# Kernel tuning notes

Hardware: AMD Instinct MI355X
Metric: run time of the kernel (lower is better)

## Reference

```python
import jax, jax.numpy as jnp
import numpy as np

D_MODEL = 1024
D_INNER = 2048
N_EXPERTS = 8
TOP_K = 2
INIT_STD = 0.02


def setup_inputs() -> dict:
    key = jax.random.key(0)
    ks = jax.random.split(key, 6)
    B, S = 2, 2048
    x = jax.random.normal(ks[0], (B, S, D_MODEL), dtype=jnp.float32)
    router_w = jax.random.normal(ks[1], (N_EXPERTS, D_MODEL), dtype=jnp.float32) * (INIT_STD * 0.1)
    router_b = jnp.zeros((N_EXPERTS,), dtype=jnp.float32)
    gate_w = jax.random.normal(ks[2], (N_EXPERTS, D_MODEL, D_INNER), dtype=jnp.float32) * INIT_STD
    up_w = jax.random.normal(ks[3], (N_EXPERTS, D_MODEL, D_INNER), dtype=jnp.float32) * INIT_STD
    down_w = jax.random.normal(ks[4], (N_EXPERTS, D_INNER, D_MODEL), dtype=jnp.float32) * INIT_STD
    return {"x": x, "router_w": router_w, "router_b": router_b,
            "gate_w": gate_w, "up_w": up_w, "down_w": down_w}


def reference(x, router_w, router_b, gate_w, up_w, down_w):
    # Router: softmax over experts, top-k, renormalize top-k probs.
    logits = jnp.einsum('bsd,ed->bse', x, router_w) + router_b          # [B,S,E]
    probs = jax.nn.softmax(logits, axis=-1)
    top_p, top_i = jax.lax.top_k(probs, TOP_K)                           # [B,S,K]
    top_p = top_p / jnp.sum(top_p, axis=-1, keepdims=True)
    # Per-expert combine weight: c[b,s,e] = sum_k top_p[b,s,k] * [top_i[b,s,k]==e]
    onehot = jax.nn.one_hot(top_i, N_EXPERTS, dtype=x.dtype)             # [B,S,K,E]
    combine = jnp.einsum('bsk,bske->bse', top_p, onehot)                 # [B,S,E]
    # SwiGLU FFN for every expert (dense form of the masked dispatch),
    # zeroed/weighted by combine coefficients.
    g = jnp.einsum('bsd,edf->ebsf', x, gate_w)                           # [E,B,S,F]
    u = jnp.einsum('bsd,edf->ebsf', x, up_w)
    h = jax.nn.silu(g) * u
    y = jnp.einsum('ebsf,efd->ebsd', h, down_w)                          # [E,B,S,D]
    out = jnp.einsum('ebsd,bse->bsd', y, combine)
    return out
```

## Files before the change

### kernel.cpp

```cpp
#include <hip/hip_runtime.h>
#include <hip/hip_bf16.h>
#include <stdint.h>

#define D_MODEL 1024
#define D_INNER 2048
#define NEXP 8
#define TOPK 2
#define BM 128
#define MAXT 72

typedef float f32x4 __attribute__((ext_vector_type(4)));
typedef short bf16x8 __attribute__((ext_vector_type(8)));

#define MEMFENCE asm volatile("" ::: "memory")

__device__ __forceinline__ unsigned short f2b(float f) {
    union { float f; uint32_t u; } v; v.f = f;
    uint32_t u = v.u;
    return (unsigned short)((u + 0x7fffu + ((u >> 16) & 1u)) >> 16);
}

__device__ __forceinline__ void gl_lds16(const void* g, void* l) {
    __builtin_amdgcn_global_load_lds((const __attribute__((address_space(1))) void*)g,
                                     (__attribute__((address_space(3))) void*)l, 16, 0, 0);
}

__global__ __launch_bounds__(256) void cast_x_kernel(
    const float* __restrict__ in, unsigned short* __restrict__ out, int n8)
{
    int i = blockIdx.x * 256 + threadIdx.x;
    if (i >= n8) return;
    const float4* p = (const float4*)(in + (size_t)i * 8);
    float4 a = p[0], b = p[1];
    unsigned short o[8] = {f2b(a.x), f2b(a.y), f2b(a.z), f2b(a.w),
                           f2b(b.x), f2b(b.y), f2b(b.z), f2b(b.w)};
    *(uint4*)(out + (size_t)i * 8) = *(uint4*)o;
}

__global__ __launch_bounds__(256) void tcast_kernel(
    const float* __restrict__ in, unsigned short* __restrict__ out, int K, int N)
{
    __shared__ unsigned short S[64][68];
    int e = blockIdx.z;
    int n0 = blockIdx.x * 64, k0 = blockIdx.y * 64;
    const float* ib = in + (size_t)e * K * N;
    unsigned short* ob = out + (size_t)e * N * K;
    int tid = threadIdx.x;
    int kk = tid >> 4, nn4 = (tid & 15) * 4;
#pragma unroll
    for (int j = 0; j < 4; j++) {
        int k = kk + 16 * j;
        float4 v = *(const float4*)&ib[(size_t)(k0 + k) * N + n0 + nn4];
        ushort4 s; s.x = f2b(v.x); s.y = f2b(v.y); s.z = f2b(v.z); s.w = f2b(v.w);
        *(ushort4*)&S[k][nn4] = s;
    }
    __syncthreads();
    int nn = tid >> 4, kk4 = (tid & 15) * 4;
#pragma unroll
    for (int j = 0; j < 4; j++) {
        int n = nn + 16 * j;
        ushort4 s;
        s.x = S[kk4 + 0][n]; s.y = S[kk4 + 1][n];
        s.z = S[kk4 + 2][n]; s.w = S[kk4 + 3][n];
        *(ushort4*)&ob[(size_t)(n0 + n) * K + k0 + kk4] = s;
    }
}

__global__ __launch_bounds__(64) void router_kernel(
    const float* __restrict__ x, const float* __restrict__ rw,
    const float* __restrict__ rb, int* __restrict__ top_i,
    float* __restrict__ top_w, int T)
{
    int t = blockIdx.x;
    if (t >= T) return;
    int l = threadIdx.x;
    float xv[16];
#pragma unroll
    for (int i = 0; i < 16; i++) xv[i] = x[(size_t)t * D_MODEL + l + 64 * i];
    float logit[NEXP];
#pragma unroll
    for (int e = 0; e < NEXP; e++) {
        float acc = 0.f;
#pragma unroll
        for (int i = 0; i < 16; i++) acc += xv[i] * rw[e * D_MODEL + l + 64 * i];
#pragma unroll
        for (int s = 32; s > 0; s >>= 1) acc += __shfl_xor(acc, s, 64);
        logit[e] = acc + rb[e];
    }
    if (l == 0) {
        int i0 = 0; float m0 = logit[0];
#pragma unroll
        for (int e = 1; e < NEXP; e++) if (logit[e] > m0) { m0 = logit[e]; i0 = e; }
        int i1 = -1; float m1 = -3.0e38f;
#pragma unroll
        for (int e = 0; e < NEXP; e++) {
            if (e == i0) continue;
            if (logit[e] > m1) { m1 = logit[e]; i1 = e; }
        }
        float w0 = 1.f / (1.f + expf(m1 - m0));
        top_i[t * 2 + 0] = i0; top_i[t * 2 + 1] = i1;
        top_w[t * 2 + 0] = w0; top_w[t * 2 + 1] = 1.f - w0;
    }
}

__global__ __launch_bounds__(256) void bucket_kernel(
    const int* __restrict__ top_i, const float* __restrict__ top_w,
    int* __restrict__ meta, int* __restrict__ tok_of_slot,
    float* __restrict__ w_of_slot, int T)
{
    __shared__ int cnt[256][NEXP];
    __shared__ int pre[256][NEXP];
    __shared__ int tot[NEXP];
    __shared__ int off[NEXP + 1];
    int tid = threadIdx.x;
    int per = (T + 255) / 256;
    int t0 = tid * per;
    for (int e = 0; e < NEXP; e++) cnt[tid][e] = 0;
    for (int t = t0; t < t0 + per && t < T; t++)
        for (int k = 0; k < TOPK; k++) cnt[tid][top_i[t * 2 + k]]++;
    __syncthreads();
    if (tid < NEXP) {
        int run = 0;
        for (int i = 0; i < 256; i++) { pre[i][tid] = run; run += cnt[i][tid]; }
        tot[tid] = run;
    }
    __syncthreads();
    if (tid == 0) {
        off[0] = 0;
        for (int e = 0; e < NEXP; e++) off[e + 1] = off[e] + tot[e];
        for (int e = 0; e <= NEXP; e++) meta[e] = off[e];
        int nt = 0;
        for (int e = 0; e < NEXP; e++)
            for (int r = off[e]; r < off[e + 1]; r += BM)
                meta[16 + nt++] = (e << 16) | r;
        for (; nt < MAXT; nt++) meta[16 + nt] = -1;
    }
    __syncthreads();
    int lc[NEXP];
#pragma unroll
    for (int e = 0; e < NEXP; e++) lc[e] = 0;
    for (int t = t0; t < t0 + per && t < T; t++) {
        for (int k = 0; k < TOPK; k++) {
            int e = top_i[t * 2 + k];
            int slot = off[e] + pre[tid][e] + lc[e]++;
            tok_of_slot[slot] = t;
            w_of_slot[slot] = top_w[t * 2 + k];
        }
    }
}

__global__ __launch_bounds__(256, 2) void moe_gate_up(
    const unsigned short* __restrict__ xb, const unsigned short* __restrict__ wgT,
    const unsigned short* __restrict__ wuT, const int* __restrict__ meta,
    const int* __restrict__ tok_of_slot, unsigned short* __restrict__ H)
{
    extern __shared__ __align__(16) unsigned short lds[];

    int lin = blockIdx.x;
    int strip = (lin & 7) * 2 + ((lin >> 3) & 1);
    int tix = lin >> 4;
    int packed = meta[16 + tix];
    if (packed < 0) return;
    int e = packed >> 16, row0 = packed & 0xffff;
    int Mloc = min(BM, meta[e + 1] - row0);
    int f0 = strip * 128;

    int tid = threadIdx.x, wv = tid >> 6, lane = tid & 63;

    const unsigned short* srcA[2];
    const unsigned short* srcG[2];
    const unsigned short* srcU[2];
#pragma unroll
    for (int j = 0; j < 2; j++) {
        int row = j * 64 + (tid >> 2);
        int p = tid & 3;
        int koffA = 8 * (p ^ ((row >> 1) & 3));
        int slot = row0 + ((row < Mloc) ? row : 0);
        srcA[j] = xb + (size_t)tok_of_slot[slot] * D_MODEL + koffA;
        size_t wb = (size_t)e * D_MODEL * D_INNER + (size_t)(f0 + row) * D_MODEL + koffA;
        srcG[j] = wgT + wb;
        srcU[j] = wuT + wb;
    }

    int wm = wv >> 1, wn = wv & 1;
    int lrow = lane & 15, kgrp = lane >> 4;
    int co = 8 * (kgrp ^ ((lrow >> 1) & 3));

    int arow[4], brow[4];
#pragma unroll
    for (int fm = 0; fm < 4; fm++) arow[fm] = (wm * 64 + fm * 16 + lrow) * 32;
#pragma unroll
    for (int fn = 0; fn < 4; fn++) brow[fn] = (wn * 64 + fn * 16 + lrow) * 32;

    f32x4 accg[4][4], accu[4][4];
#pragma unroll
    for (int i = 0; i < 4; i++)
#pragma unroll
        for (int j = 0; j < 4; j++) {
            accg[i][j] = (f32x4){0.f, 0.f, 0.f, 0.f};
            accu[i][j] = (f32x4){0.f, 0.f, 0.f, 0.f};
        }

    auto stage = [&](int u) {
        int kk = u * 32;
        unsigned short* base = lds + (u % 3) * 12288;
#pragma unroll
        for (int j = 0; j < 2; j++) {
            int d = (j * 256 + wv * 64) * 8;
            gl_lds16(srcA[j] + kk, base + d);
            gl_lds16(srcG[j] + kk, base + 4096 + d);
            gl_lds16(srcU[j] + kk, base + 8192 + d);
        }
    };

    const int NT = D_MODEL / 32;
    stage(0); stage(1);
    MEMFENCE;

    for (int t = 0; t < NT; ++t) {
        if (t + 2 < NT) stage(t + 2);
        int ahead = NT - 1 - t;
        if (ahead >= 2)      asm volatile("s_waitcnt vmcnt(12)" ::: "memory");
        else if (ahead == 1) asm volatile("s_waitcnt vmcnt(6)"  ::: "memory");
        else                 asm volatile("s_waitcnt vmcnt(0)"  ::: "memory");
        __builtin_amdgcn_s_barrier();
        MEMFENCE;

        const unsigned short* base = lds + (t % 3) * 12288;
        bf16x8 a[4], bg[4], bu[4];
#pragma unroll
        for (int fm = 0; fm < 4; fm++) a[fm] = *(const bf16x8*)(base + arow[fm] + co);
#pragma unroll
        for (int fn = 0; fn < 4; fn++) {
            bg[fn] = *(const bf16x8*)(base + 4096 + brow[fn] + co);
            bu[fn] = *(const bf16x8*)(base + 8192 + brow[fn] + co);
        }
        __builtin_amdgcn_s_setprio(1);
#pragma unroll
        for (int fm = 0; fm < 4; fm++)
#pragma unroll
            for (int fn = 0; fn < 4; fn++) {
                accg[fm][fn] = __builtin_amdgcn_mfma_f32_16x16x32_bf16(a[fm], bg[fn], accg[fm][fn], 0, 0, 0);
                accu[fm][fn] = __builtin_amdgcn_mfma_f32_16x16x32_bf16(a[fm], bu[fn], accu[fm][fn], 0, 0, 0);
            }
        __builtin_amdgcn_s_setprio(0);
        MEMFENCE;
        asm volatile("s_waitcnt lgkmcnt(0)" ::: "memory");
        __builtin_amdgcn_s_barrier();
        MEMFENCE;
    }

#pragma unroll
    for (int fm = 0; fm < 4; fm++)
#pragma unroll
        for (int fn = 0; fn < 4; fn++)
#pragma unroll
            for (int r = 0; r < 4; r++) {
                int m = wm * 64 + fm * 16 + kgrp * 4 + r;
                if (m < Mloc) {
                    int n = wn * 64 + fn * 16 + lrow;
                    float g = accg[fm][fn][r], u = accu[fm][fn][r];
                    float h = g / (1.f + __expf(-g)) * u;
                    H[(size_t)(row0 + m) * D_INNER + f0 + n] = f2b(h);
                }
            }
}

__global__ __launch_bounds__(256, 2) void moe_down(
    const unsigned short* __restrict__ H, const unsigned short* __restrict__ wdT,
    const int* __restrict__ meta, const int* __restrict__ tok_of_slot,
    const float* __restrict__ w_of_slot, float* __restrict__ out, int S2)
{
    __shared__ unsigned short lds[3 * 8192];
    __shared__ int toks[BM];
    __shared__ float wts[BM];

    int lin = blockIdx.x;
    int d0 = (lin & 7) * 128;
    int tix = lin >> 3;
    int packed = meta[16 + tix];
    if (packed < 0) return;
    int e = packed >> 16, row0 = packed & 0xffff;
    int Mloc = min(BM, meta[e + 1] - row0);

    int tid = threadIdx.x, wv = tid >> 6, lane = tid & 63;
    if (tid < BM) {
        bool v = tid < Mloc;
        toks[tid] = v ? tok_of_slot[row0 + tid] : 0;
        wts[tid] = v ? w_of_slot[row0 + tid] : 0.f;
    }

    const unsigned short* srcA[2];
    const unsigned short* srcB[2];
#pragma unroll
    for (int j = 0; j < 2; j++) {
        int row = j * 64 + (tid >> 2);
        int p = tid & 3;
        int koff = 8 * (p ^ ((row >> 1) & 3));
        int slot = min(row0 + row, S2 - 1);
        srcA[j] = H + (size_t)slot * D_INNER + koff;
        srcB[j] = wdT + (size_t)e * D_INNER * D_MODEL + (size_t)(d0 + row) * D_INNER + koff;
    }

    int wm = wv >> 1, wn = wv & 1;
    int lrow = lane & 15, kgrp = lane >> 4;
    int co = 8 * (kgrp ^ ((lrow >> 1) & 3));

    int arow[4], brow[4];
#pragma unroll
    for (int fm = 0; fm < 4; fm++) arow[fm] = (wm * 64 + fm * 16 + lrow) * 32;
#pragma unroll
    for (int fn = 0; fn < 4; fn++) brow[fn] = (wn * 64 + fn * 16 + lrow) * 32;

    f32x4 acc[4][4];
#pragma unroll
    for (int i = 0; i < 4; i++)
#pragma unroll
        for (int j = 0; j < 4; j++) acc[i][j] = (f32x4){0.f, 0.f, 0.f, 0.f};

    auto stage = [&](int u) {
        int kk = u * 32;
        unsigned short* base = lds + (u % 3) * 8192;
#pragma unroll
        for (int j = 0; j < 2; j++) {
            int d = (j * 256 + wv * 64) * 8;
            gl_lds16(srcA[j] + kk, base + d);
            gl_lds16(srcB[j] + kk, base + 4096 + d);
        }
    };

    const int NT = D_INNER / 32;
    stage(0); stage(1);
    MEMFENCE;

    for (int t = 0; t < NT; ++t) {
        if (t + 2 < NT) stage(t + 2);
        int ahead = NT - 1 - t;
        if (ahead >= 2)      asm volatile("s_waitcnt vmcnt(8)" ::: "memory");
        else if (ahead == 1) asm volatile("s_waitcnt vmcnt(4)" ::: "memory");
        else                 asm volatile("s_waitcnt vmcnt(0)" ::: "memory");
        __builtin_amdgcn_s_barrier();
        MEMFENCE;

        const unsigned short* base = lds + (t % 3) * 8192;
        bf16x8 a[4], b[4];
#pragma unroll
        for (int fm = 0; fm < 4; fm++) a[fm] = *(const bf16x8*)(base + arow[fm] + co);
#pragma unroll
        for (int fn = 0; fn < 4; fn++) b[fn] = *(const bf16x8*)(base + 4096 + brow[fn] + co);
        __builtin_amdgcn_s_setprio(1);
#pragma unroll
        for (int fm = 0; fm < 4; fm++)
#pragma unroll
            for (int fn = 0; fn < 4; fn++)
                acc[fm][fn] = __builtin_amdgcn_mfma_f32_16x16x32_bf16(a[fm], b[fn], acc[fm][fn], 0, 0, 0);
        __builtin_amdgcn_s_setprio(0);
        MEMFENCE;
        asm volatile("s_waitcnt lgkmcnt(0)" ::: "memory");
        __builtin_amdgcn_s_barrier();
        MEMFENCE;
    }

#pragma unroll
    for (int fm = 0; fm < 4; fm++)
#pragma unroll
        for (int fn = 0; fn < 4; fn++)
#pragma unroll
            for (int r = 0; r < 4; r++) {
                int m = wm * 64 + fm * 16 + kgrp * 4 + r;
                if (m < Mloc) {
                    int n = wn * 64 + fn * 16 + lrow;
                    atomicAdd(&out[(size_t)toks[m] * D_MODEL + d0 + n], wts[m] * acc[fm][fn][r]);
                }
            }
}

extern "C" void kernel_launch(void* const* d_in, const int* in_sizes, int n_in,
                              void* d_out, int out_size, void* d_ws, size_t ws_size,
                              hipStream_t stream) {
    const float* x  = (const float*)d_in[0];
    const float* rw = (const float*)d_in[1];
    const float* rb = (const float*)d_in[2];
    const float* gw = (const float*)d_in[3];
    const float* uw = (const float*)d_in[4];
    const float* dw = (const float*)d_in[5];
    float* out = (float*)d_out;

    int T = in_sizes[0] / D_MODEL;
    int S2 = 2 * T;

    char* ws = (char*)d_ws;
    size_t cur = 0;
    auto take = [&](size_t bytes) { char* p = ws + cur; cur = (cur + bytes + 255) & ~(size_t)255; return p; };
    int*   top_i = (int*)take((size_t)S2 * 4);
    float* top_w = (float*)take((size_t)S2 * 4);
    int*   meta  = (int*)take(1024);
    int*   tos   = (int*)take((size_t)S2 * 4);
    float* wos   = (float*)take((size_t)S2 * 4);
    unsigned short* xb  = (unsigned short*)take((size_t)T * D_MODEL * 2);
    unsigned short* wgT = (unsigned short*)take((size_t)NEXP * D_MODEL * D_INNER * 2);
    unsigned short* wuT = (unsigned short*)take((size_t)NEXP * D_MODEL * D_INNER * 2);
    unsigned short* wdT = (unsigned short*)take((size_t)NEXP * D_MODEL * D_INNER * 2);
    unsigned short* H   = (unsigned short*)take((size_t)S2 * D_INNER * 2);

    static const int GU_LDS = 3 * 12288 * 2;
    hipFuncSetAttribute((const void*)moe_gate_up,
                        hipFuncAttributeMaxDynamicSharedMemorySize, GU_LDS);

    hipMemsetAsync(d_out, 0, (size_t)out_size * sizeof(float), stream);

    int n8 = T * D_MODEL / 8;
    cast_x_kernel<<<(n8 + 255) / 256, 256, 0, stream>>>(x, xb, n8);
    tcast_kernel<<<dim3(D_INNER / 64, D_MODEL / 64, NEXP), 256, 0, stream>>>(gw, wgT, D_MODEL, D_INNER);
    tcast_kernel<<<dim3(D_INNER / 64, D_MODEL / 64, NEXP), 256, 0, stream>>>(uw, wuT, D_MODEL, D_INNER);
    tcast_kernel<<<dim3(D_MODEL / 64, D_INNER / 64, NEXP), 256, 0, stream>>>(dw, wdT, D_INNER, D_MODEL);

    router_kernel<<<T, 64, 0, stream>>>(x, rw, rb, top_i, top_w, T);
    bucket_kernel<<<1, 256, 0, stream>>>(top_i, top_w, meta, tos, wos, T);

    moe_gate_up<<<MAXT * 16, 256, GU_LDS, stream>>>(xb, wgT, wuT, meta, tos, H);
    moe_down<<<MAXT * 8, 256, 0, stream>>>(H, wdT, meta, tos, wos, out, S2);
}
```

Measured before the change: 273.1 us.

## Prefetch next LDS fragments, use one barrier per k-step, merge weight cast kernels

Both grouped GEMM kernels now load the next k-tile's MFMA fragments from LDS into registers right after the barrier. The MFMAs for the current tile issue first, followed by the global-to-LDS stage and a single wait-and-barrier. This drops the second per-iteration barrier and the lgkmcnt stall, at the cost of more live registers. The three weight transpose-cast launches are merged into one kernel on a 32x32x24 grid, where out-of-range blocks exit early.

After: 266.7 us. -2.4%, faster.

```diff
diff --git a/kernel.cpp b/kernel.cpp
--- a/kernel.cpp
+++ b/kernel.cpp
@@ -37,12 +37,19 @@
     *(uint4*)(out + (size_t)i * 8) = *(uint4*)o;
 }
 
-__global__ __launch_bounds__(256) void tcast_kernel(
-    const float* __restrict__ in, unsigned short* __restrict__ out, int K, int N)
+__global__ __launch_bounds__(256) void tcast3_kernel(
+    const float* __restrict__ gw, const float* __restrict__ uw, const float* __restrict__ dw,
+    unsigned short* __restrict__ gT, unsigned short* __restrict__ uT, unsigned short* __restrict__ dT)
 {
     __shared__ unsigned short S[64][68];
-    int e = blockIdx.z;
+    int which = blockIdx.z >> 3;
+    int e = blockIdx.z & 7;
+    const float* in; unsigned short* out; int K, N;
+    if (which == 0)      { in = gw; out = gT; K = D_MODEL; N = D_INNER; }
+    else if (which == 1) { in = uw; out = uT; K = D_MODEL; N = D_INNER; }
+    else                 { in = dw; out = dT; K = D_INNER; N = D_MODEL; }
     int n0 = blockIdx.x * 64, k0 = blockIdx.y * 64;
+    if (n0 >= N || k0 >= K) return;
     const float* ib = in + (size_t)e * K * N;
     unsigned short* ob = out + (size_t)e * N * K;
     int tid = threadIdx.x;
@@ -213,28 +220,28 @@
         }
     };
 
+    bf16x8 a[4], bg[4], bu[4];
+    auto load_frags = [&](int u) {
+        const unsigned short* base = lds + (u % 3) * 12288;
+#pragma unroll
+        for (int fm = 0; fm < 4; fm++) a[fm] = *(const bf16x8*)(base + arow[fm] + co);
+#pragma unroll
+        for (int fn = 0; fn < 4; fn++) {
+            bg[fn] = *(const bf16x8*)(base + 4096 + brow[fn] + co);
+            bu[fn] = *(const bf16x8*)(base + 8192 + brow[fn] + co);
+        }
+    };
+
     const int NT = D_MODEL / 32;
     stage(0); stage(1);
     MEMFENCE;
+    asm volatile("s_waitcnt vmcnt(6)" ::: "memory");
+    __builtin_amdgcn_s_barrier();
+    MEMFENCE;
+    load_frags(0);
 
     for (int t = 0; t < NT; ++t) {
-        if (t + 2 < NT) stage(t + 2);
-        int ahead = NT - 1 - t;
-        if (ahead >= 2)      asm volatile("s_waitcnt vmcnt(12)" ::: "memory");
-        else if (ahead == 1) asm volatile("s_waitcnt vmcnt(6)"  ::: "memory");
-        else                 asm volatile("s_waitcnt vmcnt(0)"  ::: "memory");
-        __builtin_amdgcn_s_barrier();
-        MEMFENCE;
-
-        const unsigned short* base = lds + (t % 3) * 12288;
-        bf16x8 a[4], bg[4], bu[4];
-#pragma unroll
-        for (int fm = 0; fm < 4; fm++) a[fm] = *(const bf16x8*)(base + arow[fm] + co);
-#pragma unroll
-        for (int fn = 0; fn < 4; fn++) {
-            bg[fn] = *(const bf16x8*)(base + 4096 + brow[fn] + co);
-            bu[fn] = *(const bf16x8*)(base + 8192 + brow[fn] + co);
-        }
+        __builtin_amdgcn_sched_barrier(0);
         __builtin_amdgcn_s_setprio(1);
 #pragma unroll
         for (int fm = 0; fm < 4; fm++)
@@ -244,10 +251,17 @@
                 accu[fm][fn] = __builtin_amdgcn_mfma_f32_16x16x32_bf16(a[fm], bu[fn], accu[fm][fn], 0, 0, 0);
             }
         __builtin_amdgcn_s_setprio(0);
-        MEMFENCE;
-        asm volatile("s_waitcnt lgkmcnt(0)" ::: "memory");
+        __builtin_amdgcn_sched_barrier(0);
+
+        if (t + 2 < NT) {
+            stage(t + 2);
+            asm volatile("s_waitcnt vmcnt(6)" ::: "memory");
+        } else if (t + 1 < NT) {
+            asm volatile("s_waitcnt vmcnt(0)" ::: "memory");
+        }
         __builtin_amdgcn_s_barrier();
         MEMFENCE;
+        if (t + 1 < NT) load_frags(t + 1);
     }
 
 #pragma unroll
@@ -329,25 +343,25 @@
         }
     };
 
+    bf16x8 a[4], b[4];
+    auto load_frags = [&](int u) {
+        const unsigned short* base = lds + (u % 3) * 8192;
+#pragma unroll
+        for (int fm = 0; fm < 4; fm++) a[fm] = *(const bf16x8*)(base + arow[fm] + co);
+#pragma unroll
+        for (int fn = 0; fn < 4; fn++) b[fn] = *(const bf16x8*)(base + 4096 + brow[fn] + co);
+    };
+
     const int NT = D_INNER / 32;
     stage(0); stage(1);
     MEMFENCE;
+    asm volatile("s_waitcnt vmcnt(4)" ::: "memory");
+    __builtin_amdgcn_s_barrier();
+    MEMFENCE;
+    load_frags(0);
 
     for (int t = 0; t < NT; ++t) {
-        if (t + 2 < NT) stage(t + 2);
-        int ahead = NT - 1 - t;
-        if (ahead >= 2)      asm volatile("s_waitcnt vmcnt(8)" ::: "memory");
-        else if (ahead == 1) asm volatile("s_waitcnt vmcnt(4)" ::: "memory");
-        else                 asm volatile("s_waitcnt vmcnt(0)" ::: "memory");
-        __builtin_amdgcn_s_barrier();
-        MEMFENCE;
-
-        const unsigned short* base = lds + (t % 3) * 8192;
-        bf16x8 a[4], b[4];
-#pragma unroll
-        for (int fm = 0; fm < 4; fm++) a[fm] = *(const bf16x8*)(base + arow[fm] + co);
-#pragma unroll
-        for (int fn = 0; fn < 4; fn++) b[fn] = *(const bf16x8*)(base + 4096 + brow[fn] + co);
+        __builtin_amdgcn_sched_barrier(0);
         __builtin_amdgcn_s_setprio(1);
 #pragma unroll
         for (int fm = 0; fm < 4; fm++)
@@ -355,10 +369,17 @@
             for (int fn = 0; fn < 4; fn++)
                 acc[fm][fn] = __builtin_amdgcn_mfma_f32_16x16x32_bf16(a[fm], b[fn], acc[fm][fn], 0, 0, 0);
         __builtin_amdgcn_s_setprio(0);
-        MEMFENCE;
-        asm volatile("s_waitcnt lgkmcnt(0)" ::: "memory");
+        __builtin_amdgcn_sched_barrier(0);
+
+        if (t + 2 < NT) {
+            stage(t + 2);
+            asm volatile("s_waitcnt vmcnt(4)" ::: "memory");
+        } else if (t + 1 < NT) {
+            asm volatile("s_waitcnt vmcnt(0)" ::: "memory");
+        }
         __builtin_amdgcn_s_barrier();
         MEMFENCE;
+        if (t + 1 < NT) load_frags(t + 1);
     }
 
 #pragma unroll
@@ -411,9 +432,7 @@
 
     int n8 = T * D_MODEL / 8;
     cast_x_kernel<<<(n8 + 255) / 256, 256, 0, stream>>>(x, xb, n8);
-    tcast_kernel<<<dim3(D_INNER / 64, D_MODEL / 64, NEXP), 256, 0, stream>>>(gw, wgT, D_MODEL, D_INNER);
-    tcast_kernel<<<dim3(D_INNER / 64, D_MODEL / 64, NEXP), 256, 0, stream>>>(uw, wuT, D_MODEL, D_INNER);
-    tcast_kernel<<<dim3(D_MODEL / 64, D_INNER / 64, NEXP), 256, 0, stream>>>(dw, wdT, D_INNER, D_MODEL);
+    tcast3_kernel<<<dim3(32, 32, 24), 256, 0, stream>>>(gw, uw, dw, wgT, wuT, wdT);
 
     router_kernel<<<T, 64, 0, stream>>>(x, rw, rb, top_i, top_w, T);
     bucket_kernel<<<1, 256, 0, stream>>>(top_i, top_w, meta, tos, wos, T);
```
